# Kernel optimization log

Hardware: AMD Instinct MI355X
Metric: run time of the kernel (lower is better)

The kernel has to match this reference:

```python
import jax, jax.numpy as jnp
import numpy as np

B, H, S, Dqk, Dv = 4, 16, 2048, 64, 64
HID = 1024  # hidden_dim; v_tot_dim = H*Dv = 1024


def setup_inputs() -> dict:
    key = jax.random.key(0)
    kq, kk, kv, kw = jax.random.split(key, 4)
    return {
        "q": jax.random.normal(kq, (B, H, S, Dqk), dtype=jnp.float32),
        "k": jax.random.normal(kk, (B, H, S, Dqk), dtype=jnp.float32),
        "v": jax.random.normal(kv, (B, H, S, Dv), dtype=jnp.float32),
        "attention_mask": jnp.zeros((B, H, S, S), dtype=jnp.float32),
        "W_proj": jax.random.normal(kw, (HID, H * Dv), dtype=jnp.float32) * 0.02,
    }


def reference(q, k, v, attention_mask, W_proj):
    # scores: [B, H, S, S] -- explicitly materialized, as in the original
    scores = jnp.einsum("bhqd,bhkd->bhqk", q, k) + attention_mask
    attn = jax.nn.softmax(scores, axis=-1)
    # attn @ v -> [B, H, S, Dv]
    out = jnp.einsum("bhqk,bhkd->bhqd", attn, v)
    # rearrange '... h l d -> ... l (h d)'
    out = jnp.transpose(out, (0, 2, 1, 3)).reshape(B, S, H * Dv)
    # Linear(bias=False): y = x @ W^T
    out = out @ W_proj.T
    return (out, attn)
```

## Files before the change

### kernel.cpp

```cpp
#include <hip/hip_runtime.h>
#include <hip/hip_bf16.h>

#define BB 4
#define HH 16
#define SS 2048
#define DD 64
#define HIDD 1024
#define NBH (BB * HH)
#define EQK (NBH * SS * DD)
#define LOG2E 1.44269504088896f
#define M2C 57.7078016f

typedef __attribute__((ext_vector_type(4))) float f32x4;
typedef __attribute__((ext_vector_type(8))) short bf16x8;

__device__ __forceinline__ short f2bf(float x) {
    union { float f; unsigned u; } v; v.f = x;
    return (short)((v.u + 0x7FFFu + ((v.u >> 16) & 1u)) >> 16);
}
__device__ __forceinline__ float bf2f(short b) {
    union { float f; unsigned u; } v;
    v.u = ((unsigned)(unsigned short)b) << 16;
    return v.f;
}
__device__ __forceinline__ int pk2(float a, float b) {
    return ((int)(unsigned short)f2bf(b) << 16) | (int)(unsigned short)f2bf(a);
}
__device__ __forceinline__ f32x4 mfma16(bf16x8 a, bf16x8 b, f32x4 c) {
    return __builtin_amdgcn_mfma_f32_16x16x32_bf16(a, b, c, 0, 0, 0);
}
__device__ __forceinline__ float fexp2(float x) { return __builtin_amdgcn_exp2f(x); }

__global__ __launch_bounds__(256) void prep_split(const float* __restrict__ k,
                                                  short* __restrict__ hi,
                                                  short* __restrict__ lo) {
    int t = blockIdx.x * 256 + threadIdx.x;
    int lane = t & 63, h = (t >> 6) & 1, kt = (t >> 7) & 127, bh = t >> 14;
    int r16 = lane & 15, gl = lane >> 4;
    int s = kt * 16 + r16, d0 = h * 32 + gl * 8;
    const float* src = k + ((size_t)bh * SS + s) * DD + d0;
    bf16x8 hh, ll;
#pragma unroll
    for (int j = 0; j < 8; ++j) {
        float x = src[j];
        short hb = f2bf(x);
        hh[j] = hb;
        ll[j] = f2bf(x - bf2f(hb));
    }
    *(bf16x8*)(hi + (size_t)t * 8) = hh;
    *(bf16x8*)(lo + (size_t)t * 8) = ll;
}

__global__ __launch_bounds__(256) void prep_cast(const float* __restrict__ src,
                                                 short* __restrict__ dst, int n8) {
    int i = blockIdx.x * 256 + threadIdx.x;
    if (i >= n8) return;
    const float* p = src + (size_t)i * 8;
    bf16x8 h;
#pragma unroll
    for (int j = 0; j < 8; ++j) h[j] = f2bf(p[j]);
    *(bf16x8*)(dst + (size_t)i * 8) = h;
}

__global__ __launch_bounds__(256) void vt_kernel(const float* __restrict__ v,
                                                 short* __restrict__ vT) {
    int t = blockIdx.x * 256 + threadIdx.x;
    int lane = t & 63, cc = (t >> 6) & 63, dt = (t >> 12) & 3, bh = t >> 14;
    int r16 = lane & 15, gl = lane >> 4;
    const float* src = v + ((size_t)bh * SS + cc * 32 + gl * 8) * DD + dt * 16 + r16;
    bf16x8 o;
#pragma unroll
    for (int j = 0; j < 8; ++j) o[j] = f2bf(src[(size_t)j * DD]);
    *(bf16x8*)(vT + (size_t)t * 8) = o;
}

template <int PLAN>
__global__ __launch_bounds__(256, 2) void attn_sweep(
    const float* __restrict__ q,
    const short* __restrict__ khi, const short* __restrict__ klo,
    const float* __restrict__ mask, const short* __restrict__ vT,
    short* __restrict__ Pout, float* __restrict__ attn_raw,
    float* __restrict__ lrow, short* __restrict__ pvb16) {
    const int w = threadIdx.x >> 6;
    const int lane = threadIdx.x & 63;
    const int r16 = lane & 15, g = lane >> 4;
    const int bid = blockIdx.x;
    const int swz = (bid & 7) * 256 + (bid >> 3);
    const int bh = swz >> 5;
    const int q0 = (swz & 31) * 64 + w * 16;

    const float* qrow = q + ((size_t)bh * SS + q0 + r16) * DD + g * 8;
    bf16x8 qh0, ql0, qh1, ql1;
#pragma unroll
    for (int j = 0; j < 8; ++j) {
        float x0 = qrow[j];
        short h0 = f2bf(x0); qh0[j] = h0; ql0[j] = f2bf(x0 - bf2f(h0));
        float x1 = qrow[32 + j];
        short h1 = f2bf(x1); qh1[j] = h1; ql1[j] = f2bf(x1 - bf2f(h1));
    }

    const short* kb = khi + (size_t)bh * 131072;
    const short* lb = klo + (size_t)bh * 131072;
    const float* mrow = mask + ((size_t)bh * SS + q0 + r16) * SS;
    const short* vtb = vT + (size_t)bh * 131072;
    short* Pb = Pout + ((size_t)bh * SS + q0 + r16) * SS;
    float* ab = attn_raw + ((size_t)bh * SS + q0 + r16) * SS;

    float lsum = 0.f;
    f32x4 opv0 = {0.f,0.f,0.f,0.f}, opv1 = {0.f,0.f,0.f,0.f};
    f32x4 opv2 = {0.f,0.f,0.f,0.f}, opv3 = {0.f,0.f,0.f,0.f};

    auto LKK = [&](bf16x8 (&KH)[4], bf16x8 (&KL)[4], int ccv) {
        const short* kc = kb + (size_t)ccv * 2048 + lane * 8;
        const short* lc = lb + (size_t)ccv * 2048 + lane * 8;
        KH[0] = *(const bf16x8*)(kc);        KH[1] = *(const bf16x8*)(kc + 512);
        KH[2] = *(const bf16x8*)(kc + 1024); KH[3] = *(const bf16x8*)(kc + 1536);
        KL[0] = *(const bf16x8*)(lc);        KL[1] = *(const bf16x8*)(lc + 512);
        KL[2] = *(const bf16x8*)(lc + 1024); KL[3] = *(const bf16x8*)(lc + 1536);
    };

    auto BODY = [&](bf16x8 (&KH)[4], bf16x8 (&KL)[4], float4 mk0, float4 mk1, int ccv) {
        const short* vc = vtb + (size_t)ccv * 512 + lane * 8;
        bf16x8 vf0 = *(const bf16x8*)(vc);
        bf16x8 vf1 = *(const bf16x8*)(vc + 32768);
        bf16x8 vf2 = *(const bf16x8*)(vc + 65536);
        bf16x8 vf3 = *(const bf16x8*)(vc + 98304);
        f32x4 c00 = {mk0.x, mk0.y, mk0.z, mk0.w};
        f32x4 c10 = {mk1.x, mk1.y, mk1.z, mk1.w};
        f32x4 c01 = {0.f,0.f,0.f,0.f}, c11 = {0.f,0.f,0.f,0.f};
        c00 = mfma16(KH[0], qh0, c00);  c01 = mfma16(KH[1], qh1, c01);
        c10 = mfma16(KH[2], qh0, c10);  c11 = mfma16(KH[3], qh1, c11);
        c00 = mfma16(KL[0], qh0, c00);  c01 = mfma16(KL[1], qh1, c01);
        c10 = mfma16(KL[2], qh0, c10);  c11 = mfma16(KL[3], qh1, c11);
        c00 = mfma16(KH[0], ql0, c00);  c01 = mfma16(KH[1], ql1, c01);
        c10 = mfma16(KH[2], ql0, c10);  c11 = mfma16(KH[3], ql1, c11);
        float p0[4], p1[4];
#pragma unroll
        for (int i = 0; i < 4; ++i) {
            p0[i] = fexp2(__builtin_fmaf(c00[i] + c01[i], LOG2E, -M2C));
            p1[i] = fexp2(__builtin_fmaf(c10[i] + c11[i], LOG2E, -M2C));
        }
        lsum += (p0[0] + p0[1]) + (p0[2] + p0[3]) + (p1[0] + p1[1]) + (p1[2] + p1[3]);
        if constexpr (PLAN == 1) {
            float4 s0 = {p0[0], p0[1], p0[2], p0[3]};
            float4 s1 = {p1[0], p1[1], p1[2], p1[3]};
            *(float4*)(ab + ccv * 32 + 4 * g) = s0;
            *(float4*)(ab + ccv * 32 + 16 + 4 * g) = s1;
        }
        int e0 = pk2(p0[0], p0[1]), e1 = pk2(p0[2], p0[3]);
        int e2 = pk2(p1[0], p1[1]), e3 = pk2(p1[2], p1[3]);
        int f0 = __shfl_xor(e0, 16), f1 = __shfl_xor(e1, 16);
        int f2 = __shfl_xor(e2, 16), f3 = __shfl_xor(e3, 16);
        const bool ge = (g & 1) == 0;
        int L0 = ge ? e0 : f0, L1 = ge ? e1 : f1, L2 = ge ? f0 : e0, L3 = ge ? f1 : e1;
        int H0 = ge ? e2 : f2, H1 = ge ? e3 : f3, H2 = ge ? f2 : e2, H3 = ge ? f3 : e3;
        const bool lo2 = g < 2;
        int r0 = __shfl_xor(lo2 ? H0 : L0, 32);
        int r1 = __shfl_xor(lo2 ? H1 : L1, 32);
        int r2 = __shfl_xor(lo2 ? H2 : L2, 32);
        int r3 = __shfl_xor(lo2 ? H3 : L3, 32);
        union { int i4[4]; bf16x8 v; } ua;
        ua.i4[0] = (g == 0) ? L0 : (g == 3) ? H0 : r0;
        ua.i4[1] = (g == 0) ? L1 : (g == 3) ? H1 : r1;
        ua.i4[2] = (g == 0) ? L2 : (g == 3) ? H2 : r2;
        ua.i4[3] = (g == 0) ? L3 : (g == 3) ? H3 : r3;
        bf16x8 pf = ua.v;
        if constexpr (PLAN == 0) {
            *(bf16x8*)(Pb + ccv * 32 + g * 8) = pf;
        }
        opv0 = mfma16(pf, vf0, opv0);
        opv1 = mfma16(pf, vf1, opv1);
        opv2 = mfma16(pf, vf2, opv2);
        opv3 = mfma16(pf, vf3, opv3);
    };

    float4 MM[8][2];
#pragma unroll
    for (int b = 0; b < 8; ++b) {
        const float* mp = mrow + b * 32 + 4 * g;
        MM[b][0] = *(const float4*)(mp);
        MM[b][1] = *(const float4*)(mp + 16);
    }
    bf16x8 KH_[2][4], KL_[2][4];
    LKK(KH_[0], KL_[0], 0);

    for (int it = 0; it < 8; ++it) {
        const int cc0 = it * 8;
#pragma unroll
        for (int b = 0; b < 8; ++b) {
            const int ccv = cc0 + b;
            const int cur = b & 1, nxt = cur ^ 1;
            const int knb = (ccv + 1 < 64) ? ccv + 1 : 63;
            LKK(KH_[nxt], KL_[nxt], knb);
            float4 m0 = MM[b][0], m1 = MM[b][1];
            const int mnb = (ccv + 8 < 64) ? ccv + 8 : 63;
            const float* mp = mrow + mnb * 32 + 4 * g;
            MM[b][0] = *(const float4*)(mp);
            MM[b][1] = *(const float4*)(mp + 16);
            BODY(KH_[cur], KL_[cur], m0, m1, ccv);
        }
    }

    lsum += __shfl_xor(lsum, 16);
    lsum += __shfl_xor(lsum, 32);
    const float linv = 1.0f / lsum;
    if (g == 0) lrow[(size_t)bh * SS + q0 + r16] = linv;

    short* pvo = pvb16 + ((size_t)bh * SS + q0) * DD;
#pragma unroll
    for (int i = 0; i < 4; ++i) {
        float li = __shfl(linv, 4 * g + i, 64);
        pvo[(size_t)(4 * g + i) * DD + 0  + r16] = f2bf(opv0[i] * li);
        pvo[(size_t)(4 * g + i) * DD + 16 + r16] = f2bf(opv1[i] * li);
        pvo[(size_t)(4 * g + i) * DD + 32 + r16] = f2bf(opv2[i] * li);
        pvo[(size_t)(4 * g + i) * DD + 48 + r16] = f2bf(opv3[i] * li);
    }
}

__global__ __launch_bounds__(256) void rescale_a(const short* __restrict__ P,
                                                 const float* __restrict__ lrow,
                                                 float* __restrict__ attn) {
    size_t t = (size_t)blockIdx.x * 256 + threadIdx.x;
    size_t row = t >> 8;
    int c0 = (int)(t & 255) << 3;
    float s = lrow[row];
    bf16x8 p = *(const bf16x8*)(P + row * SS + c0);
    float4 o0, o1;
    o0.x = bf2f(p[0]) * s; o0.y = bf2f(p[1]) * s; o0.z = bf2f(p[2]) * s; o0.w = bf2f(p[3]) * s;
    o1.x = bf2f(p[4]) * s; o1.y = bf2f(p[5]) * s; o1.z = bf2f(p[6]) * s; o1.w = bf2f(p[7]) * s;
    float* d = attn + row * SS + c0;
    *(float4*)d = o0;
    *(float4*)(d + 4) = o1;
}

__global__ __launch_bounds__(256) void rescale_b(float* __restrict__ attn,
                                                 const float* __restrict__ lrow) {
    size_t t = (size_t)blockIdx.x * 256 + threadIdx.x;
    size_t row = t >> 8;
    int c0 = (int)(t & 255) << 3;
    float s = lrow[row];
    float* d = attn + row * SS + c0;
    float4 a = *(float4*)d, b = *(float4*)(d + 4);
    a.x *= s; a.y *= s; a.z *= s; a.w *= s;
    b.x *= s; b.y *= s; b.z *= s; b.w *= s;
    *(float4*)d = a;
    *(float4*)(d + 4) = b;
}

__global__ __launch_bounds__(256) void proj_kernel(const short* __restrict__ xb,
                                                   const short* __restrict__ wb,
                                                   float* __restrict__ out) {
    const int w = threadIdx.x >> 6;
    const int lane = threadIdx.x & 63;
    const int r16 = lane & 15, g = lane >> 4;
    const int ww = blockIdx.x * 4 + w;
    const int nb = ww >> 4;
    const int ob = ww & 15;
    const int n0 = nb * 16;
    const int n = n0 + r16;
    const int b = n >> 11, s = n & (SS - 1);

    f32x4 acc[4];
#pragma unroll
    for (int ot = 0; ot < 4; ++ot) acc[ot] = f32x4{0.f, 0.f, 0.f, 0.f};

    for (int kk = 0; kk < HIDD / 32; ++kk) {
        const int c = kk * 32 + g * 8;
        const int h = c >> 6, d = c & 63;
        bf16x8 af = *(const bf16x8*)(xb + ((size_t)(b * HH + h) * SS + s) * DD + d);
#pragma unroll
        for (int ot = 0; ot < 4; ++ot) {
            const int o = (ob * 64) + ot * 16 + r16;
            bf16x8 bf = *(const bf16x8*)(wb + (size_t)o * HIDD + c);
            acc[ot] = mfma16(af, bf, acc[ot]);
        }
    }
#pragma unroll
    for (int ot = 0; ot < 4; ++ot)
#pragma unroll
        for (int i = 0; i < 4; ++i)
            out[(size_t)(n0 + g * 4 + i) * HIDD + (ob * 64) + ot * 16 + r16] = acc[ot][i];
}

extern "C" void kernel_launch(void* const* d_in, const int* in_sizes, int n_in,
                              void* d_out, int out_size, void* d_ws, size_t ws_size,
                              hipStream_t stream) {
    const float* q   = (const float*)d_in[0];
    const float* k   = (const float*)d_in[1];
    const float* v   = (const float*)d_in[2];
    const float* msk = (const float*)d_in[3];
    const float* Wp  = (const float*)d_in[4];

    float* out = (float*)d_out;
    float* attn_out = out + (size_t)BB * SS * HIDD;

    char* ws = (char*)d_ws;
    size_t off = 0;
    short* vT  = (short*)(ws + off); off += (size_t)EQK * 2;
    short* khi = (short*)(ws + off); off += (size_t)EQK * 2;
    short* klo = (short*)(ws + off); off += (size_t)EQK * 2;
    short* wbf = (short*)(ws + off); off += (size_t)HIDD * HIDD * 2;
    short* pvb = (short*)(ws + off); off += (size_t)EQK * 2;
    float* lrw = (float*)(ws + off); off += (size_t)NBH * SS * 4;
    short* Pbf = (short*)(ws + off);
    size_t needA = off + (size_t)NBH * SS * SS * 2;
    const bool planA = (ws_size >= needA);

    prep_split<<<EQK / 8 / 256, 256, 0, stream>>>(k, khi, klo);
    prep_cast<<<HIDD * HIDD / 8 / 256, 256, 0, stream>>>(Wp, wbf, HIDD * HIDD / 8);
    vt_kernel<<<EQK / 8 / 256, 256, 0, stream>>>(v, vT);

    const int rsblocks = (int)(((size_t)NBH * SS * SS / 8) / 256);
    if (planA) {
        attn_sweep<0><<<NBH * (SS / 64), 256, 0, stream>>>(
            q, khi, klo, msk, vT, Pbf, (float*)ws, lrw, pvb);
        rescale_a<<<rsblocks, 256, 0, stream>>>(Pbf, lrw, attn_out);
    } else {
        attn_sweep<1><<<NBH * (SS / 64), 256, 0, stream>>>(
            q, khi, klo, msk, vT, (short*)ws, attn_out, lrw, pvb);
        rescale_b<<<rsblocks, 256, 0, stream>>>(attn_out, lrw);
    }
    proj_kernel<<<(BB * SS / 16) * (HIDD / 64) / 4, 256, 0, stream>>>(pvb, wbf, out);
}
```

Measured before the change: 1.064 ms.

## Split attention sweep into score/exp pass and fused PV-plus-rescale pass

Moves the P·V matmul out of the score sweep into a second kernel that also does the normalization rescale of the attention matrix, replacing the separate rescale kernels. The first kernel becomes lighter (no V loads, no cross-lane shuffles, no K double-buffering) and runs with higher occupancy. The second kernel reads P once and uses it both for the rescaled attn write and for the MFMA with V, so the standalone rescale pass and its extra read of P disappear. The price is that the sweep loses explicit K prefetch, and the mask is now added after the MFMA instead of being used as the accumulator seed, so rounding may differ slightly.

New measurement: 1.239 ms. +16.4%, slower.

```diff
diff --git a/kernel.cpp b/kernel.cpp
--- a/kernel.cpp
+++ b/kernel.cpp
@@ -13,6 +13,7 @@
 
 typedef __attribute__((ext_vector_type(4))) float f32x4;
 typedef __attribute__((ext_vector_type(8))) short bf16x8;
+typedef __attribute__((ext_vector_type(2))) int i32x2;
 
 __device__ __forceinline__ short f2bf(float x) {
     union { float f; unsigned u; } v; v.f = x;
@@ -75,12 +76,12 @@
 }
 
 template <int PLAN>
-__global__ __launch_bounds__(256, 2) void attn_sweep(
+__global__ __launch_bounds__(256, 4) void sweep_lite(
     const float* __restrict__ q,
     const short* __restrict__ khi, const short* __restrict__ klo,
-    const float* __restrict__ mask, const short* __restrict__ vT,
+    const float* __restrict__ mask,
     short* __restrict__ Pout, float* __restrict__ attn_raw,
-    float* __restrict__ lrow, short* __restrict__ pvb16) {
+    float* __restrict__ lrow) {
     const int w = threadIdx.x >> 6;
     const int lane = threadIdx.x & 63;
     const int r16 = lane & 15, g = lane >> 4;
@@ -102,109 +103,125 @@
     const short* kb = khi + (size_t)bh * 131072;
     const short* lb = klo + (size_t)bh * 131072;
     const float* mrow = mask + ((size_t)bh * SS + q0 + r16) * SS;
-    const short* vtb = vT + (size_t)bh * 131072;
     short* Pb = Pout + ((size_t)bh * SS + q0 + r16) * SS;
     float* ab = attn_raw + ((size_t)bh * SS + q0 + r16) * SS;
 
     float lsum = 0.f;
+
+    auto BODY = [&](float4 mk0, float4 mk1, int ccv) {
+        const short* kc = kb + (size_t)ccv * 2048 + lane * 8;
+        const short* lc = lb + (size_t)ccv * 2048 + lane * 8;
+        bf16x8 KH0 = *(const bf16x8*)(kc);        bf16x8 KH1 = *(const bf16x8*)(kc + 512);
+        bf16x8 KH2 = *(const bf16x8*)(kc + 1024); bf16x8 KH3 = *(const bf16x8*)(kc + 1536);
+        bf16x8 KL0 = *(const bf16x8*)(lc);        bf16x8 KL1 = *(const bf16x8*)(lc + 512);
+        bf16x8 KL2 = *(const bf16x8*)(lc + 1024); bf16x8 KL3 = *(const bf16x8*)(lc + 1536);
+        f32x4 c00 = {0.f,0.f,0.f,0.f}, c10 = {0.f,0.f,0.f,0.f};
+        f32x4 c01 = {0.f,0.f,0.f,0.f}, c11 = {0.f,0.f,0.f,0.f};
+        c00 = mfma16(KH0, qh0, c00);  c01 = mfma16(KH1, qh1, c01);
+        c10 = mfma16(KH2, qh0, c10);  c11 = mfma16(KH3, qh1, c11);
+        c00 = mfma16(KL0, qh0, c00);  c01 = mfma16(KL1, qh1, c01);
+        c10 = mfma16(KL2, qh0, c10);  c11 = mfma16(KL3, qh1, c11);
+        c00 = mfma16(KH0, ql0, c00);  c01 = mfma16(KH1, ql1, c01);
+        c10 = mfma16(KH2, ql0, c10);  c11 = mfma16(KH3, ql1, c11);
+        float p0[4], p1[4];
+        float mk0a[4] = {mk0.x, mk0.y, mk0.z, mk0.w};
+        float mk1a[4] = {mk1.x, mk1.y, mk1.z, mk1.w};
+#pragma unroll
+        for (int i = 0; i < 4; ++i) {
+            p0[i] = fexp2(__builtin_fmaf(c00[i] + c01[i] + mk0a[i], LOG2E, -M2C));
+            p1[i] = fexp2(__builtin_fmaf(c10[i] + c11[i] + mk1a[i], LOG2E, -M2C));
+        }
+        lsum += (p0[0] + p0[1]) + (p0[2] + p0[3]) + (p1[0] + p1[1]) + (p1[2] + p1[3]);
+        if constexpr (PLAN == 0) {
+            i32x2 s0 = {pk2(p0[0], p0[1]), pk2(p0[2], p0[3])};
+            i32x2 s1 = {pk2(p1[0], p1[1]), pk2(p1[2], p1[3])};
+            *(i32x2*)(Pb + ccv * 32 + 4 * g) = s0;
+            *(i32x2*)(Pb + ccv * 32 + 16 + 4 * g) = s1;
+        } else {
+            float4 s0 = {p0[0], p0[1], p0[2], p0[3]};
+            float4 s1 = {p1[0], p1[1], p1[2], p1[3]};
+            *(float4*)(ab + ccv * 32 + 4 * g) = s0;
+            *(float4*)(ab + ccv * 32 + 16 + 4 * g) = s1;
+        }
+    };
+
+    float4 MM[2][2];
+#pragma unroll
+    for (int b = 0; b < 2; ++b) {
+        const float* mp = mrow + b * 32 + 4 * g;
+        MM[b][0] = *(const float4*)(mp);
+        MM[b][1] = *(const float4*)(mp + 16);
+    }
+    for (int cc = 0; cc < 64; cc += 2) {
+#pragma unroll
+        for (int b = 0; b < 2; ++b) {
+            float4 m0 = MM[b][0], m1 = MM[b][1];
+            const int nb = cc + b + 2;
+            const float* mp = mrow + (nb < 64 ? nb : 63) * 32 + 4 * g;
+            MM[b][0] = *(const float4*)(mp);
+            MM[b][1] = *(const float4*)(mp + 16);
+            BODY(m0, m1, cc + b);
+        }
+    }
+
+    lsum += __shfl_xor(lsum, 16);
+    lsum += __shfl_xor(lsum, 32);
+    if (g == 0) lrow[(size_t)bh * SS + q0 + r16] = 1.0f / lsum;
+}
+
+template <int PLAN>
+__global__ __launch_bounds__(256, 4) void pv_rescale(
+    const short* __restrict__ P, float* __restrict__ attn,
+    const float* __restrict__ lrow, const short* __restrict__ vT,
+    short* __restrict__ pvb16) {
+    const int w = threadIdx.x >> 6;
+    const int lane = threadIdx.x & 63;
+    const int r16 = lane & 15, g = lane >> 4;
+    const int bid = blockIdx.x;
+    const int swz = (bid & 7) * 256 + (bid >> 3);
+    const int bh = swz >> 5;
+    const int q0 = (swz & 31) * 64 + w * 16;
+
+    const float linv = lrow[(size_t)bh * SS + q0 + r16];
+    const short* Pb = P + ((size_t)bh * SS + q0 + r16) * SS;
+    float* ab = attn + ((size_t)bh * SS + q0 + r16) * SS;
+    const short* vtb = vT + (size_t)bh * 131072;
+
     f32x4 opv0 = {0.f,0.f,0.f,0.f}, opv1 = {0.f,0.f,0.f,0.f};
     f32x4 opv2 = {0.f,0.f,0.f,0.f}, opv3 = {0.f,0.f,0.f,0.f};
 
-    auto LKK = [&](bf16x8 (&KH)[4], bf16x8 (&KL)[4], int ccv) {
-        const short* kc = kb + (size_t)ccv * 2048 + lane * 8;
-        const short* lc = lb + (size_t)ccv * 2048 + lane * 8;
-        KH[0] = *(const bf16x8*)(kc);        KH[1] = *(const bf16x8*)(kc + 512);
-        KH[2] = *(const bf16x8*)(kc + 1024); KH[3] = *(const bf16x8*)(kc + 1536);
-        KL[0] = *(const bf16x8*)(lc);        KL[1] = *(const bf16x8*)(lc + 512);
-        KL[2] = *(const bf16x8*)(lc + 1024); KL[3] = *(const bf16x8*)(lc + 1536);
-    };
-
-    auto BODY = [&](bf16x8 (&KH)[4], bf16x8 (&KL)[4], float4 mk0, float4 mk1, int ccv) {
-        const short* vc = vtb + (size_t)ccv * 512 + lane * 8;
+    for (int cc = 0; cc < 64; ++cc) {
+        const short* vc = vtb + (size_t)cc * 512 + lane * 8;
         bf16x8 vf0 = *(const bf16x8*)(vc);
         bf16x8 vf1 = *(const bf16x8*)(vc + 32768);
         bf16x8 vf2 = *(const bf16x8*)(vc + 65536);
         bf16x8 vf3 = *(const bf16x8*)(vc + 98304);
-        f32x4 c00 = {mk0.x, mk0.y, mk0.z, mk0.w};
-        f32x4 c10 = {mk1.x, mk1.y, mk1.z, mk1.w};
-        f32x4 c01 = {0.f,0.f,0.f,0.f}, c11 = {0.f,0.f,0.f,0.f};
-        c00 = mfma16(KH[0], qh0, c00);  c01 = mfma16(KH[1], qh1, c01);
-        c10 = mfma16(KH[2], qh0, c10);  c11 = mfma16(KH[3], qh1, c11);
-        c00 = mfma16(KL[0], qh0, c00);  c01 = mfma16(KL[1], qh1, c01);
-        c10 = mfma16(KL[2], qh0, c10);  c11 = mfma16(KL[3], qh1, c11);
-        c00 = mfma16(KH[0], ql0, c00);  c01 = mfma16(KH[1], ql1, c01);
-        c10 = mfma16(KH[2], ql0, c10);  c11 = mfma16(KH[3], ql1, c11);
-        float p0[4], p1[4];
-#pragma unroll
-        for (int i = 0; i < 4; ++i) {
-            p0[i] = fexp2(__builtin_fmaf(c00[i] + c01[i], LOG2E, -M2C));
-            p1[i] = fexp2(__builtin_fmaf(c10[i] + c11[i], LOG2E, -M2C));
-        }
-        lsum += (p0[0] + p0[1]) + (p0[2] + p0[3]) + (p1[0] + p1[1]) + (p1[2] + p1[3]);
-        if constexpr (PLAN == 1) {
-            float4 s0 = {p0[0], p0[1], p0[2], p0[3]};
-            float4 s1 = {p1[0], p1[1], p1[2], p1[3]};
-            *(float4*)(ab + ccv * 32 + 4 * g) = s0;
-            *(float4*)(ab + ccv * 32 + 16 + 4 * g) = s1;
-        }
-        int e0 = pk2(p0[0], p0[1]), e1 = pk2(p0[2], p0[3]);
-        int e2 = pk2(p1[0], p1[1]), e3 = pk2(p1[2], p1[3]);
-        int f0 = __shfl_xor(e0, 16), f1 = __shfl_xor(e1, 16);
-        int f2 = __shfl_xor(e2, 16), f3 = __shfl_xor(e3, 16);
-        const bool ge = (g & 1) == 0;
-        int L0 = ge ? e0 : f0, L1 = ge ? e1 : f1, L2 = ge ? f0 : e0, L3 = ge ? f1 : e1;
-        int H0 = ge ? e2 : f2, H1 = ge ? e3 : f3, H2 = ge ? f2 : e2, H3 = ge ? f3 : e3;
-        const bool lo2 = g < 2;
-        int r0 = __shfl_xor(lo2 ? H0 : L0, 32);
-        int r1 = __shfl_xor(lo2 ? H1 : L1, 32);
-        int r2 = __shfl_xor(lo2 ? H2 : L2, 32);
-        int r3 = __shfl_xor(lo2 ? H3 : L3, 32);
-        union { int i4[4]; bf16x8 v; } ua;
-        ua.i4[0] = (g == 0) ? L0 : (g == 3) ? H0 : r0;
-        ua.i4[1] = (g == 0) ? L1 : (g == 3) ? H1 : r1;
-        ua.i4[2] = (g == 0) ? L2 : (g == 3) ? H2 : r2;
-        ua.i4[3] = (g == 0) ? L3 : (g == 3) ? H3 : r3;
-        bf16x8 pf = ua.v;
+        bf16x8 pf;
         if constexpr (PLAN == 0) {
-            *(bf16x8*)(Pb + ccv * 32 + g * 8) = pf;
+            pf = *(const bf16x8*)(Pb + cc * 32 + g * 8);
+            float4 o0, o1;
+            o0.x = bf2f(pf[0]) * linv; o0.y = bf2f(pf[1]) * linv;
+            o0.z = bf2f(pf[2]) * linv; o0.w = bf2f(pf[3]) * linv;
+            o1.x = bf2f(pf[4]) * linv; o1.y = bf2f(pf[5]) * linv;
+            o1.z = bf2f(pf[6]) * linv; o1.w = bf2f(pf[7]) * linv;
+            float* d = ab + cc * 32 + g * 8;
+            *(float4*)d = o0;
+            *(float4*)(d + 4) = o1;
+        } else {
+            float* d = ab + cc * 32 + g * 8;
+            float4 a = *(float4*)d, b = *(float4*)(d + 4);
+            pf[0] = f2bf(a.x); pf[1] = f2bf(a.y); pf[2] = f2bf(a.z); pf[3] = f2bf(a.w);
+            pf[4] = f2bf(b.x); pf[5] = f2bf(b.y); pf[6] = f2bf(b.z); pf[7] = f2bf(b.w);
+            a.x *= linv; a.y *= linv; a.z *= linv; a.w *= linv;
+            b.x *= linv; b.y *= linv; b.z *= linv; b.w *= linv;
+            *(float4*)d = a;
+            *(float4*)(d + 4) = b;
         }
         opv0 = mfma16(pf, vf0, opv0);
         opv1 = mfma16(pf, vf1, opv1);
         opv2 = mfma16(pf, vf2, opv2);
         opv3 = mfma16(pf, vf3, opv3);
-    };
-
-    float4 MM[8][2];
-#pragma unroll
-    for (int b = 0; b < 8; ++b) {
-        const float* mp = mrow + b * 32 + 4 * g;
-        MM[b][0] = *(const float4*)(mp);
-        MM[b][1] = *(const float4*)(mp + 16);
-    }
-    bf16x8 KH_[2][4], KL_[2][4];
-    LKK(KH_[0], KL_[0], 0);
-
-    for (int it = 0; it < 8; ++it) {
-        const int cc0 = it * 8;
-#pragma unroll
-        for (int b = 0; b < 8; ++b) {
-            const int ccv = cc0 + b;
-            const int cur = b & 1, nxt = cur ^ 1;
-            const int knb = (ccv + 1 < 64) ? ccv + 1 : 63;
-            LKK(KH_[nxt], KL_[nxt], knb);
-            float4 m0 = MM[b][0], m1 = MM[b][1];
-            const int mnb = (ccv + 8 < 64) ? ccv + 8 : 63;
-            const float* mp = mrow + mnb * 32 + 4 * g;
-            MM[b][0] = *(const float4*)(mp);
-            MM[b][1] = *(const float4*)(mp + 16);
-            BODY(KH_[cur], KL_[cur], m0, m1, ccv);
-        }
-    }
-
-    lsum += __shfl_xor(lsum, 16);
-    lsum += __shfl_xor(lsum, 32);
-    const float linv = 1.0f / lsum;
-    if (g == 0) lrow[(size_t)bh * SS + q0 + r16] = linv;
+    }
 
     short* pvo = pvb16 + ((size_t)bh * SS + q0) * DD;
 #pragma unroll
@@ -215,36 +232,6 @@
         pvo[(size_t)(4 * g + i) * DD + 32 + r16] = f2bf(opv2[i] * li);
         pvo[(size_t)(4 * g + i) * DD + 48 + r16] = f2bf(opv3[i] * li);
     }
-}
-
-__global__ __launch_bounds__(256) void rescale_a(const short* __restrict__ P,
-                                                 const float* __restrict__ lrow,
-                                                 float* __restrict__ attn) {
-    size_t t = (size_t)blockIdx.x * 256 + threadIdx.x;
-    size_t row = t >> 8;
-    int c0 = (int)(t & 255) << 3;
-    float s = lrow[row];
-    bf16x8 p = *(const bf16x8*)(P + row * SS + c0);
-    float4 o0, o1;
-    o0.x = bf2f(p[0]) * s; o0.y = bf2f(p[1]) * s; o0.z = bf2f(p[2]) * s; o0.w = bf2f(p[3]) * s;
-    o1.x = bf2f(p[4]) * s; o1.y = bf2f(p[5]) * s; o1.z = bf2f(p[6]) * s; o1.w = bf2f(p[7]) * s;
-    float* d = attn + row * SS + c0;
-    *(float4*)d = o0;
-    *(float4*)(d + 4) = o1;
-}
-
-__global__ __launch_bounds__(256) void rescale_b(float* __restrict__ attn,
-                                                 const float* __restrict__ lrow) {
-    size_t t = (size_t)blockIdx.x * 256 + threadIdx.x;
-    size_t row = t >> 8;
-    int c0 = (int)(t & 255) << 3;
-    float s = lrow[row];
-    float* d = attn + row * SS + c0;
-    float4 a = *(float4*)d, b = *(float4*)(d + 4);
-    a.x *= s; a.y *= s; a.z *= s; a.w *= s;
-    b.x *= s; b.y *= s; b.z *= s; b.w *= s;
-    *(float4*)d = a;
-    *(float4*)(d + 4) = b;
 }
 
 __global__ __launch_bounds__(256) void proj_kernel(const short* __restrict__ xb,
@@ -310,15 +297,16 @@
     prep_cast<<<HIDD * HIDD / 8 / 256, 256, 0, stream>>>(Wp, wbf, HIDD * HIDD / 8);
     vt_kernel<<<EQK / 8 / 256, 256, 0, stream>>>(v, vT);
 
-    const int rsblocks = (int)(((size_t)NBH * SS * SS / 8) / 256);
     if (planA) {
-        attn_sweep<0><<<NBH * (SS / 64), 256, 0, stream>>>(
-            q, khi, klo, msk, vT, Pbf, (float*)ws, lrw, pvb);
-        rescale_a<<<rsblocks, 256, 0, stream>>>(Pbf, lrw, attn_out);
+        sweep_lite<0><<<NBH * (SS / 64), 256, 0, stream>>>(
+            q, khi, klo, msk, Pbf, (float*)ws, lrw);
+        pv_rescale<0><<<NBH * (SS / 64), 256, 0, stream>>>(
+            Pbf, attn_out, lrw, vT, pvb);
     } else {
-        attn_sweep<1><<<NBH * (SS / 64), 256, 0, stream>>>(
-            q, khi, klo, msk, vT, (short*)ws, attn_out, lrw, pvb);
-        rescale_b<<<rsblocks, 256, 0, stream>>>(attn_out, lrw);
+        sweep_lite<1><<<NBH * (SS / 64), 256, 0, stream>>>(
+            q, khi, klo, msk, (short*)ws, attn_out, lrw);
+        pv_rescale<1><<<NBH * (SS / 64), 256, 0, stream>>>(
+            (short*)ws, attn_out, lrw, vT, pvb);
     }
     proj_kernel<<<(BB * SS / 16) * (HIDD / 64) / 4, 256, 0, stream>>>(pvb, wbf, out);
 }
```
